# Optimization experiments

Hardware: AMD Instinct MI355X
Metric: run time of the kernel (lower is better)

The kernel has to match this reference:

```python
import jax, jax.numpy as jnp
import numpy as np

N = 100000   # nodes
E = 300000   # directed edges
D = 256      # emb_dim
G = 4000     # graphs
L = 5        # num_layer
F_IN = 40    # num_atom_features
NUM_BOND_TYPE = 6       # pretrain-gnns convention; self-loop bond type = 4
NUM_BOND_DIRECTION = 3
EPS = 1e-5


def setup_inputs() -> dict:
    key = jax.random.key(0)
    ks = jax.random.split(key, 32)
    s = 0.05
    inp = {}
    inp["x"] = jax.random.normal(ks[0], (N, F_IN), jnp.float32)
    inp["edge_index"] = jax.random.randint(ks[1], (2, E), 0, N)
    inp["edge_attr"] = jax.random.randint(ks[2], (E, 2), 0, 3)
    inp["batch"] = jnp.sort(jax.random.randint(ks[3], (N,), 0, G))
    # atom embedding (Linear + ReLU)
    inp["embW"] = jax.random.normal(ks[4], (F_IN, D), jnp.float32) * s
    inp["embB"] = jnp.zeros((D,), jnp.float32)
    # per-layer GINConv params (stacked over layers)
    inp["ee1"] = jax.random.normal(ks[5], (L, NUM_BOND_TYPE, D), jnp.float32) * s
    inp["ee2"] = jax.random.normal(ks[6], (L, NUM_BOND_DIRECTION, D), jnp.float32) * s
    inp["W1"] = jax.random.normal(ks[7], (L, D, 2 * D), jnp.float32) * s
    inp["b1"] = jnp.zeros((L, 2 * D), jnp.float32)
    inp["W2"] = jax.random.normal(ks[8], (L, 2 * D, D), jnp.float32) * s
    inp["b2"] = jnp.zeros((L, D), jnp.float32)
    inp["bn_g"] = jnp.ones((L, D), jnp.float32)
    inp["bn_b"] = jnp.zeros((L, D), jnp.float32)
    # MLP head: 256 -> 256 -> 128 -> 64 -> 32 -> 1
    dims = [D, D, D // 2, D // 4, D // 8]
    kk = jax.random.split(ks[9], 5)
    for i in range(4):
        inp[f"hW{i}"] = jax.random.normal(kk[i], (dims[i], dims[i + 1]), jnp.float32) * s
        inp[f"hb{i}"] = jnp.zeros((dims[i + 1],), jnp.float32)
    inp["hWo"] = jax.random.normal(kk[4], (dims[4], 1), jnp.float32) * s
    inp["hbo"] = jnp.zeros((1,), jnp.float32)
    return inp


def reference(x, edge_index, edge_attr, batch, embW, embB, ee1, ee2, W1, b1, W2, b2,
              bn_g, bn_b, hW0, hb0, hW1, hb1, hW2, hb2, hW3, hb3, hWo, hbo):
    src, dst = edge_index[0], edge_index[1]
    ea0, ea1 = edge_attr[:, 0], edge_attr[:, 1]
    # x_embedding1: Linear + ReLU
    h = jax.nn.relu(x @ embW + embB)
    for l in range(L):
        # GINConv: gather source features + edge embeddings, scatter-add to dst
        msg = h[src] + ee1[l][ea0] + ee2[l][ea1]        # [E, D]
        agg = jax.ops.segment_sum(msg, dst, num_segments=N)
        # self-loop message (bond type 4, direction 0)
        agg = agg + h + ee1[l][4] + ee2[l][0]
        # GIN MLP: Linear(D, 2D) -> ReLU -> Linear(2D, D)
        h2 = jax.nn.relu(agg @ W1[l] + b1[l]) @ W2[l] + b2[l]
        # BatchNorm1d (training-mode batch statistics, biased variance)
        mu = h2.mean(axis=0)
        var = h2.var(axis=0)
        h2 = (h2 - mu) * jax.lax.rsqrt(var + EPS) * bn_g[l] + bn_b[l]
        if l < L - 1:
            h2 = jax.nn.relu(h2)
        # dropout with drop_ratio=0.0 -> identity
        h = h2
    # JK == 'last'
    node_rep = h
    # global_mean_pool
    counts = jnp.maximum(jax.ops.segment_sum(jnp.ones((N,), node_rep.dtype), batch, num_segments=G), 1.0)
    mol = jax.ops.segment_sum(node_rep, batch, num_segments=G) / counts[:, None]
    # MLP head
    z = jax.nn.relu(mol @ hW0 + hb0)
    z = jax.nn.relu(z @ hW1 + hb1)
    z = jax.nn.relu(z @ hW2 + hb2)
    z = jax.nn.relu(z @ hW3 + hb3)
    out = z @ hWo + hbo
    return out.reshape(-1)  # MolEmbed.view(-1), num_tasks == 1
```

## Files before the change

### kernel.cpp

```cpp
#include <hip/hip_runtime.h>
#include <hip/hip_bf16.h>

#define NN 100000
#define EE 300000
#define GG 4000
#define LL 5
#define GPB 4
#define SC_CHUNK 1024
#define SC_NB ((NN + SC_CHUNK - 1) / SC_CHUNK)

typedef _Float16 half8  __attribute__((ext_vector_type(8)));
typedef _Float16 half4v __attribute__((ext_vector_type(4)));
typedef float    f32x4  __attribute__((ext_vector_type(4)));

__device__ inline short f2h(float f) {
    _Float16 h = (_Float16)f;
    short s; __builtin_memcpy(&s, &h, 2); return s;
}

__device__ inline void async_load16(const void* g, void* l) {
    __builtin_amdgcn_global_load_lds(
        (const __attribute__((address_space(1))) unsigned int*)g,
        (__attribute__((address_space(3))) unsigned int*)l, 16, 0, 0);
}

__global__ __launch_bounds__(256) void k_count(
    int* __restrict__ deg, const int* __restrict__ ei)
{
    int e = blockIdx.x * 256 + threadIdx.x;
    if (e < EE) atomicAdd(&deg[ei[EE + e]], 1);
}

__global__ __launch_bounds__(256) void k_scan_partial(
    int* __restrict__ partial, const int* __restrict__ deg)
{
    int b = blockIdx.x, t = threadIdx.x;
    int lane = t & 63, w = t >> 6;
    int base = b * SC_CHUNK + t * 4;
    int s = 0;
#pragma unroll
    for (int j = 0; j < 4; ++j) {
        int i = base + j;
        if (i < NN) s += deg[i];
    }
#pragma unroll
    for (int off = 1; off < 64; off <<= 1) s += __shfl_xor(s, off, 64);
    __shared__ int ws[4];
    if (lane == 0) ws[w] = s;
    __syncthreads();
    if (t == 0) partial[b] = ws[0] + ws[1] + ws[2] + ws[3];
}

__global__ __launch_bounds__(128) void k_scan_base(
    int* __restrict__ bases, int* __restrict__ offs, const int* __restrict__ partial)
{
    int t = threadIdx.x;
    int lane = t & 63, w = t >> 6;
    int p = (t < SC_NB) ? partial[t] : 0;
    int x = p;
#pragma unroll
    for (int off = 1; off < 64; off <<= 1) {
        int nb = __shfl_up(x, off, 64);
        if (lane >= off) x += nb;
    }
    __shared__ int w0tot;
    if (t == 63) w0tot = x;
    __syncthreads();
    if (w == 1) x += w0tot;
    if (t < SC_NB) bases[t] = x - p;
    if (t == 0) offs[NN] = EE;
}

__global__ __launch_bounds__(256) void k_scan_final(
    int* __restrict__ offs, int* __restrict__ cursor,
    const int* __restrict__ deg, const int* __restrict__ bases)
{
    int b = blockIdx.x, t = threadIdx.x;
    int lane = t & 63, w = t >> 6;
    int base = b * SC_CHUNK + t * 4;
    int v[4], pre[4], run = 0;
#pragma unroll
    for (int j = 0; j < 4; ++j) {
        int i = base + j;
        v[j] = (i < NN) ? deg[i] : 0;
        pre[j] = run;
        run += v[j];
    }
    int x = run;
#pragma unroll
    for (int off = 1; off < 64; off <<= 1) {
        int nb = __shfl_up(x, off, 64);
        if (lane >= off) x += nb;
    }
    int tex = x - run;
    __shared__ int ws[4];
    if (lane == 63) ws[w] = x;
    __syncthreads();
    int woff = 0;
    for (int k = 0; k < 4; ++k) if (k < w) woff += ws[k];
    int tbase = bases[b] + woff + tex;
#pragma unroll
    for (int j = 0; j < 4; ++j) {
        int i = base + j;
        if (i < NN) { offs[i] = tbase + pre[j]; cursor[i] = tbase + pre[j]; }
    }
}

__global__ __launch_bounds__(256) void k_fill(
    int* __restrict__ csr, int* __restrict__ cursor,
    const int* __restrict__ ei, const int* __restrict__ ea)
{
    int e = blockIdx.x * 256 + threadIdx.x;
    if (e >= EE) return;
    int s = ei[e];
    int d = ei[EE + e];
    int c = ea[2 * e] * 3 + ea[2 * e + 1];
    int slot = atomicAdd(&cursor[d], 1);
    csr[slot] = s | (c << 20);
}

__global__ __launch_bounds__(256) void k_goffs(
    int* __restrict__ goffs, const int* __restrict__ batch)
{
    int n = blockIdx.x * 256 + threadIdx.x;
    if (n >= NN) return;
    int b = batch[n];
    int bp = (n == 0) ? -1 : batch[n - 1];
    for (int g = bp + 1; g <= b; ++g) goffs[g] = n;
    if (n == NN - 1)
        for (int g = b + 1; g <= GG; ++g) goffs[g] = NN;
}

__global__ __launch_bounds__(256) void k_combo(
    float* __restrict__ tbl, const float* __restrict__ ee1, const float* __restrict__ ee2)
{
    int c = blockIdx.x;
    int l = blockIdx.y;
    int t = threadIdx.x;
    int i1 = (c < 9) ? c / 3 : 4;
    int i2 = (c < 9) ? c % 3 : 0;
    tbl[((size_t)l * 10 + c) * 256 + t] =
        ee1[((size_t)l * 6 + i1) * 256 + t] + ee2[((size_t)l * 3 + i2) * 256 + t];
}

__global__ __launch_bounds__(256) void k_pack_emb(
    _Float16* __restrict__ Wep, const float* __restrict__ embW)
{
    int idx = blockIdx.x * 256 + threadIdx.x;
    int ks = idx >> 13, r = idx & 8191;
    int n = r >> 5, kk = r & 31;
    int k = ks * 32 + kk;
    float v = (k < 40) ? embW[(size_t)k * 256 + n] : 0.f;
    Wep[idx] = (_Float16)v;
}

__global__ __launch_bounds__(256) void k_embed_mfma(
    _Float16* __restrict__ H, const float* __restrict__ x,
    const _Float16* __restrict__ Wep, const float* __restrict__ bias)
{
    __shared__ __align__(16) char smem[67584];
    _Float16* As = (_Float16*)smem;
    _Float16* Bs = (_Float16*)(smem + 16384);
    _Float16* Cs = (_Float16*)smem;

    const int t = threadIdx.x;
    const int w = t >> 6, lane = t & 63;
    const int quad = lane >> 4, l16 = lane & 15;
    const int wr = w >> 1, wc = w & 1;
    const int gm0 = blockIdx.x * 128;

#pragma unroll
    for (int i = 0; i < 8; ++i) {
        int u = i * 256 + t;
        async_load16((const char*)Wep + u * 16, (char*)Bs + u * 16);
    }

    {
        int row = t >> 1, half = t & 1;
        int rg = gm0 + row; if (rg > NN - 1) rg = NN - 1;
        const float* xp = x + (size_t)rg * 40 + half * 20;
        float v[20];
#pragma unroll
        for (int j = 0; j < 5; ++j) {
            float4 q = *(const float4*)(xp + j * 4);
            v[j * 4 + 0] = q.x; v[j * 4 + 1] = q.y; v[j * 4 + 2] = q.z; v[j * 4 + 3] = q.w;
        }
#pragma unroll
        for (int j = 0; j < 20; ++j) {
            int col = half * 20 + j;
            int ks = col >> 5, kk = col & 31;
            As[ks * 4096 + row * 32 + kk] = (_Float16)v[j];
        }
        int kb = 8 + half * 12;
#pragma unroll
        for (int j = 0; j < 12; ++j)
            As[4096 + row * 32 + kb + j] = (_Float16)0.f;
    }

    float biasreg[8];
#pragma unroll
    for (int nt = 0; nt < 8; ++nt)
        biasreg[nt] = bias[wc * 128 + nt * 16 + l16];

    f32x4 acc[4][8];
#pragma unroll
    for (int i = 0; i < 4; ++i)
#pragma unroll
        for (int j = 0; j < 8; ++j) acc[i][j] = (f32x4){0.f, 0.f, 0.f, 0.f};

    __syncthreads();

#pragma unroll
    for (int ks = 0; ks < 2; ++ks) {
        half8 af[4], bfr[8];
#pragma unroll
        for (int mt = 0; mt < 4; ++mt)
            af[mt] = *(const half8*)(As + ks * 4096 + (wr * 64 + mt * 16 + l16) * 32 + quad * 8);
#pragma unroll
        for (int nt = 0; nt < 8; ++nt)
            bfr[nt] = *(const half8*)(Bs + ks * 8192 + (wc * 128 + nt * 16 + l16) * 32 + quad * 8);
#pragma unroll
        for (int mt = 0; mt < 4; ++mt)
#pragma unroll
            for (int nt = 0; nt < 8; ++nt)
                acc[mt][nt] = __builtin_amdgcn_mfma_f32_16x16x32_f16(
                    af[mt], bfr[nt], acc[mt][nt], 0, 0, 0);
    }

    __syncthreads();
#pragma unroll
    for (int mt = 0; mt < 4; ++mt)
#pragma unroll
        for (int nt = 0; nt < 8; ++nt)
#pragma unroll
            for (int r = 0; r < 4; ++r) {
                int row = wr * 64 + mt * 16 + quad * 4 + r;
                int col = wc * 128 + nt * 16 + l16;
                Cs[row * 264 + col] = (_Float16)fmaxf(acc[mt][nt][r] + biasreg[nt], 0.f);
            }
    __syncthreads();
#pragma unroll
    for (int i = 0; i < 16; ++i) {
        int u = i * 256 + t;
        int m = u >> 5, ch = u & 31;
        int grow = gm0 + m;
        if (grow < NN)
            *(int4*)(H + (size_t)grow * 256 + ch * 8) =
                *(const int4*)(Cs + m * 264 + ch * 8);
    }
}

template <int AFF>
__global__ __launch_bounds__(256) void k_aggregate(
    _Float16* __restrict__ agg, const _Float16* __restrict__ hin,
    const int* __restrict__ offs, const int* __restrict__ csr,
    const float* __restrict__ tbl,
    const float* __restrict__ scale, const float* __restrict__ shift)
{
    int t = threadIdx.x;
    int w = t >> 6, lane = t & 63;
    int n = blockIdx.x * 4 + w;

    f32x4 sc, sh;
    if (AFF) { sc = ((const f32x4*)scale)[lane]; sh = ((const f32x4*)shift)[lane]; }
    const f32x4* tb4 = (const f32x4*)tbl;

    half4v hv = *(const half4v*)(hin + (size_t)n * 256 + lane * 4);
    f32x4 acc = tb4[9 * 64 + lane];
#pragma unroll
    for (int i = 0; i < 4; ++i) {
        float v = (float)hv[i];
        if (AFF) v = fmaf(v, sc[i], sh[i]);
        acc[i] += fmaxf(v, 0.f);
    }

    int o0 = offs[n], o1 = offs[n + 1];
    for (int j = o0; j < o1; ++j) {
        int entry = csr[j];
        int s = entry & 0xFFFFF;
        int c = entry >> 20;
        half4v gv = *(const half4v*)(hin + (size_t)s * 256 + lane * 4);
        f32x4 tv = tb4[c * 64 + lane];
#pragma unroll
        for (int i = 0; i < 4; ++i) {
            float v = (float)gv[i];
            if (AFF) v = fmaf(v, sc[i], sh[i]);
            acc[i] += fmaxf(v, 0.f) + tv[i];
        }
    }

    half4v o;
#pragma unroll
    for (int i = 0; i < 4; ++i) o[i] = (_Float16)acc[i];
    *(half4v*)(agg + (size_t)n * 256 + lane * 4) = o;
}

__global__ __launch_bounds__(256) void k_pack(
    short* __restrict__ dst, const float* __restrict__ src, int K, int Nsz)
{
    int nb = blockIdx.x, kb = blockIdx.y, l = blockIdx.z;
    int t = threadIdx.x;
    __shared__ float T[32][65];
    const float* s = src + ((size_t)l * K + kb * 32) * Nsz + nb * 64;
#pragma unroll
    for (int i = 0; i < 8; ++i) {
        int idx = i * 256 + t;
        int kk = idx >> 6, nl = idx & 63;
        T[kk][nl] = s[(size_t)kk * Nsz + nl];
    }
    __syncthreads();
    int nl = t >> 2, kq = t & 3;
    union { short s[8]; int4 v; } o;
#pragma unroll
    for (int j = 0; j < 8; ++j) o.s[j] = f2h(T[kq * 8 + j][nl]);
    short* d = dst + (((size_t)l * (K / 32) + kb) * Nsz + nb * 64 + nl) * 32 + kq * 8;
    *(int4*)d = o.v;
}

__global__ __launch_bounds__(256, 3) void k_fused_mlp(
    _Float16* __restrict__ H2, const _Float16* __restrict__ A,
    const short* __restrict__ W1p, const float* __restrict__ b1,
    const short* __restrict__ W2p, const float* __restrict__ b2,
    float* __restrict__ stats)
{
    __shared__ __align__(16) char smem[49152];
    _Float16* As = (_Float16*)smem;
    _Float16* Us = (_Float16*)(smem + 32768);
    _Float16* Cs = (_Float16*)smem;

    const int t = threadIdx.x;
    const int w = t >> 6, lane = t & 63;
    const int quad = lane >> 4, l16 = lane & 15;
    const int bm = blockIdx.x;
    const int gm0 = bm * 64;
    const int swz = l16 & 7;

#pragma unroll
    for (int i = 0; i < 8; ++i) {
        int u = i * 256 + t;
        int row = u >> 5;
        int gcol = (u & 31) ^ (row & 7);
        int grow = gm0 + row; if (grow > NN - 1) grow = NN - 1;
        async_load16(A + (size_t)grow * 256 + gcol * 8, (char*)As + u * 16);
    }

    const _Float16* w1w = (const _Float16*)W1p + ((size_t)(w * 32 + l16)) * 32 + quad * 8;
    const _Float16* w2w = (const _Float16*)W2p + ((size_t)(w * 64 + l16)) * 32 + quad * 8;

    half8 a1p[2];
#pragma unroll
    for (int ct = 0; ct < 2; ++ct)
        a1p[ct] = *(const half8*)(w1w + (size_t)(ct * 16) * 32);

    f32x4 acc2[4][4];
#pragma unroll
    for (int i = 0; i < 4; ++i)
#pragma unroll
        for (int j = 0; j < 4; ++j) acc2[i][j] = (f32x4){0.f, 0.f, 0.f, 0.f};

    __syncthreads();

    for (int j = 0; j < 4; ++j) {
        f32x4 acc1[2][4];
#pragma unroll
        for (int a = 0; a < 2; ++a)
#pragma unroll
            for (int b = 0; b < 4; ++b) acc1[a][b] = (f32x4){0.f, 0.f, 0.f, 0.f};

#pragma unroll
        for (int kb = 0; kb < 8; ++kb) {
            half8 a1c[2];
            a1c[0] = a1p[0]; a1c[1] = a1p[1];
            if (kb < 7) {
#pragma unroll
                for (int ct = 0; ct < 2; ++ct)
                    a1p[ct] = *(const half8*)(w1w +
                        ((size_t)(kb + 1) * 512 + j * 128 + ct * 16) * 32);
            }
            int slotA = (kb * 4 + quad) ^ swz;
            half8 b1f[4];
#pragma unroll
            for (int urt = 0; urt < 4; ++urt)
                b1f[urt] = *(const half8*)(As + (urt * 16 + l16) * 256 + slotA * 8);
#pragma unroll
            for (int ct = 0; ct < 2; ++ct)
#pragma unroll
                for (int urt = 0; urt < 4; ++urt)
                    acc1[ct][urt] = __builtin_amdgcn_mfma_f32_16x16x32_f16(
                        a1c[ct], b1f[urt], acc1[ct][urt], 0, 0, 0);
        }

        half8 a2p[4];
#pragma unroll
        for (int nt = 0; nt < 4; ++nt)
            a2p[nt] = *(const half8*)(w2w + ((size_t)(j * 4) * 256 + nt * 16) * 32);

#pragma unroll
        for (int ct = 0; ct < 2; ++ct) {
            int ucl = w * 32 + ct * 16 + quad * 4;
            float4 bv = *(const float4*)(b1 + j * 128 + ucl);
            int G = ucl >> 3;
            int hs = quad & 1;
#pragma unroll
            for (int urt = 0; urt < 4; ++urt) {
                int ur = urt * 16 + l16;
                int S = G ^ (ur & 7);
                half4v o;
                o[0] = (_Float16)fmaxf(acc1[ct][urt][0] + bv.x, 0.f);
                o[1] = (_Float16)fmaxf(acc1[ct][urt][1] + bv.y, 0.f);
                o[2] = (_Float16)fmaxf(acc1[ct][urt][2] + bv.z, 0.f);
                o[3] = (_Float16)fmaxf(acc1[ct][urt][3] + bv.w, 0.f);
                *(half4v*)(Us + ur * 128 + S * 8 + hs * 4) = o;
            }
        }
        asm volatile("s_waitcnt lgkmcnt(0)" ::: "memory");
        __builtin_amdgcn_s_barrier();
        __builtin_amdgcn_sched_barrier(0);

#pragma unroll
        for (int kk = 0; kk < 4; ++kk) {
            half8 a2c[4];
#pragma unroll
            for (int nt = 0; nt < 4; ++nt) a2c[nt] = a2p[nt];
            if (kk < 3) {
#pragma unroll
                for (int nt = 0; nt < 4; ++nt)
                    a2p[nt] = *(const half8*)(w2w +
                        ((size_t)(j * 4 + kk + 1) * 256 + nt * 16) * 32);
            } else if (j < 3) {
#pragma unroll
                for (int ct = 0; ct < 2; ++ct)
                    a1p[ct] = *(const half8*)(w1w +
                        ((size_t)(j + 1) * 128 + ct * 16) * 32);
            }
            int slotU = (kk * 4 + quad) ^ swz;
            half8 b2f[4];
#pragma unroll
            for (int mt = 0; mt < 4; ++mt)
                b2f[mt] = *(const half8*)(Us + (mt * 16 + l16) * 128 + slotU * 8);
#pragma unroll
            for (int nt = 0; nt < 4; ++nt)
#pragma unroll
                for (int mt = 0; mt < 4; ++mt)
                    acc2[nt][mt] = __builtin_amdgcn_mfma_f32_16x16x32_f16(
                        a2c[nt], b2f[mt], acc2[nt][mt], 0, 0, 0);
        }
        asm volatile("s_waitcnt lgkmcnt(0)" ::: "memory");
        __builtin_amdgcn_s_barrier();
        __builtin_amdgcn_sched_barrier(0);
    }

    int slot2 = bm & 63;
#pragma unroll
    for (int nt = 0; nt < 4; ++nt) {
        int nb = w * 64 + nt * 16 + quad * 4;
        float4 bv = *(const float4*)(b2 + nb);
        float s1[4] = {0.f, 0.f, 0.f, 0.f};
        float s2[4] = {0.f, 0.f, 0.f, 0.f};
#pragma unroll
        for (int mt = 0; mt < 4; ++mt) {
            int mr = mt * 16 + l16;
            int m = gm0 + mr;
            float v0 = acc2[nt][mt][0] + bv.x;
            float v1 = acc2[nt][mt][1] + bv.y;
            float v2 = acc2[nt][mt][2] + bv.z;
            float v3 = acc2[nt][mt][3] + bv.w;
            half4v o;
            o[0] = (_Float16)v0; o[1] = (_Float16)v1;
            o[2] = (_Float16)v2; o[3] = (_Float16)v3;
            *(half4v*)(Cs + mr * 264 + nb) = o;
            if (m < NN) {
                s1[0] += v0; s1[1] += v1; s1[2] += v2; s1[3] += v3;
                s2[0] += v0 * v0; s2[1] += v1 * v1;
                s2[2] += v2 * v2; s2[3] += v3 * v3;
            }
        }
#pragma unroll
        for (int r = 0; r < 4; ++r) {
            s1[r] += __shfl_xor(s1[r], 1, 64); s2[r] += __shfl_xor(s2[r], 1, 64);
            s1[r] += __shfl_xor(s1[r], 2, 64); s2[r] += __shfl_xor(s2[r], 2, 64);
            s1[r] += __shfl_xor(s1[r], 4, 64); s2[r] += __shfl_xor(s2[r], 4, 64);
            s1[r] += __shfl_xor(s1[r], 8, 64); s2[r] += __shfl_xor(s2[r], 8, 64);
            if (l16 == 0) {
                atomicAdd(&stats[slot2 * 512 + nb + r], s1[r]);
                atomicAdd(&stats[slot2 * 512 + 256 + nb + r], s2[r]);
            }
        }
    }
    __syncthreads();
#pragma unroll
    for (int i = 0; i < 8; ++i) {
        int u = i * 256 + t;
        int m = u >> 5, ch = u & 31;
        int grow = gm0 + m;
        if (grow < NN)
            *(int4*)(H2 + (size_t)grow * 256 + ch * 8) =
                *(const int4*)(Cs + m * 264 + ch * 8);
    }
}

__global__ __launch_bounds__(256) void k_bn_finalize(
    float* __restrict__ scale, float* __restrict__ shift,
    float* __restrict__ stats,
    const float* __restrict__ bn_g, const float* __restrict__ bn_b)
{
    int t = threadIdx.x;
    float s1 = 0.f, s2 = 0.f;
    for (int j = 0; j < 64; ++j) {
        s1 += stats[j * 512 + t];
        s2 += stats[j * 512 + 256 + t];
        stats[j * 512 + t] = 0.f;
        stats[j * 512 + 256 + t] = 0.f;
    }
    float mu  = s1 / (float)NN;
    float var = s2 / (float)NN - mu * mu;
    float sc  = bn_g[t] * rsqrtf(var + 1e-5f);
    scale[t] = sc;
    shift[t] = bn_b[t] - mu * sc;
}

__global__ __launch_bounds__(256) void k_pool(
    float* __restrict__ mol, const _Float16* __restrict__ h,
    const int* __restrict__ goffs,
    const float* __restrict__ scale, const float* __restrict__ shift)
{
    int g = blockIdx.x;
    int t = threadIdx.x;
    int s = goffs[g], e = goffs[g + 1];
    float sum = 0.f;
    for (int n = s; n < e; ++n) sum += (float)h[(size_t)n * 256 + t];
    int c = e - s; if (c < 1) c = 1;
    mol[(size_t)g * 256 + t] = fmaf(sum / (float)c, scale[t], shift[t]);
}

__global__ __launch_bounds__(256) void k_head(
    float* __restrict__ out, const float* __restrict__ mol,
    const float* __restrict__ hW0, const float* __restrict__ hb0,
    const float* __restrict__ hW1, const float* __restrict__ hb1,
    const float* __restrict__ hW2, const float* __restrict__ hb2,
    const float* __restrict__ hW3, const float* __restrict__ hb3,
    const float* __restrict__ hWo, const float* __restrict__ hbo)
{
    __shared__ float za[GPB][256];
    __shared__ float zb[GPB][256];
    const int t = threadIdx.x;
    const int g0 = blockIdx.x * GPB;

#pragma unroll
    for (int g = 0; g < GPB; ++g)
        za[g][t] = mol[(size_t)(g0 + g) * 256 + t];
    __syncthreads();

    {
        float acc[GPB];
#pragma unroll
        for (int g = 0; g < GPB; ++g) acc[g] = 0.f;
        for (int k = 0; k < 256; ++k) {
            float w = hW0[k * 256 + t];
#pragma unroll
            for (int g = 0; g < GPB; ++g) acc[g] = fmaf(za[g][k], w, acc[g]);
        }
        float b = hb0[t];
#pragma unroll
        for (int g = 0; g < GPB; ++g) zb[g][t] = fmaxf(acc[g] + b, 0.f);
    }
    __syncthreads();

    if (t < 128) {
        float acc[GPB];
#pragma unroll
        for (int g = 0; g < GPB; ++g) acc[g] = 0.f;
        for (int k = 0; k < 256; ++k) {
            float w = hW1[k * 128 + t];
#pragma unroll
            for (int g = 0; g < GPB; ++g) acc[g] = fmaf(zb[g][k], w, acc[g]);
        }
        float b = hb1[t];
#pragma unroll
        for (int g = 0; g < GPB; ++g) za[g][t] = fmaxf(acc[g] + b, 0.f);
    }
    __syncthreads();

    if (t < 64) {
        float acc[GPB];
#pragma unroll
        for (int g = 0; g < GPB; ++g) acc[g] = 0.f;
        for (int k = 0; k < 128; ++k) {
            float w = hW2[k * 64 + t];
#pragma unroll
            for (int g = 0; g < GPB; ++g) acc[g] = fmaf(za[g][k], w, acc[g]);
        }
        float b = hb2[t];
#pragma unroll
        for (int g = 0; g < GPB; ++g) zb[g][t] = fmaxf(acc[g] + b, 0.f);
    }
    __syncthreads();

    if (t < 32) {
        float acc[GPB];
#pragma unroll
        for (int g = 0; g < GPB; ++g) acc[g] = 0.f;
        for (int k = 0; k < 64; ++k) {
            float w = hW3[k * 32 + t];
#pragma unroll
            for (int g = 0; g < GPB; ++g) acc[g] = fmaf(zb[g][k], w, acc[g]);
        }
        float b = hb3[t];
#pragma unroll
        for (int g = 0; g < GPB; ++g) za[g][t] = fmaxf(acc[g] + b, 0.f);
    }
    __syncthreads();

    if (t < GPB) {
        float s = hbo[0];
        for (int k = 0; k < 32; ++k) s = fmaf(za[t][k], hWo[k], s);
        out[g0 + t] = s;
    }
}

extern "C" void kernel_launch(void* const* d_in, const int* in_sizes, int n_in,
                              void* d_out, int out_size, void* d_ws, size_t ws_size,
                              hipStream_t stream)
{
    const float* x    = (const float*)d_in[0];
    const int*   ei   = (const int*)d_in[1];
    const int*   ea   = (const int*)d_in[2];
    const int*   batch= (const int*)d_in[3];
    const float* embW = (const float*)d_in[4];
    const float* embB = (const float*)d_in[5];
    const float* ee1  = (const float*)d_in[6];
    const float* ee2  = (const float*)d_in[7];
    const float* W1   = (const float*)d_in[8];
    const float* b1   = (const float*)d_in[9];
    const float* W2   = (const float*)d_in[10];
    const float* b2   = (const float*)d_in[11];
    const float* bng  = (const float*)d_in[12];
    const float* bnb  = (const float*)d_in[13];
    const float* hW0  = (const float*)d_in[14];
    const float* hb0  = (const float*)d_in[15];
    const float* hW1  = (const float*)d_in[16];
    const float* hb1  = (const float*)d_in[17];
    const float* hW2  = (const float*)d_in[18];
    const float* hb2  = (const float*)d_in[19];
    const float* hW3  = (const float*)d_in[20];
    const float* hb3  = (const float*)d_in[21];
    const float* hWo  = (const float*)d_in[22];
    const float* hbo  = (const float*)d_in[23];
    float* out = (float*)d_out;

    char* ws = (char*)d_ws;
    size_t off = 0;
    _Float16* h2buf = (_Float16*)(ws + off); off += (size_t)NN * 256 * 2;
    _Float16* aggbuf= (_Float16*)(ws + off); off += (size_t)NN * 256 * 2;
    short* W1p      = (short*)(ws + off);    off += (size_t)5 * 131072 * 2;
    short* W2p      = (short*)(ws + off);    off += (size_t)5 * 131072 * 2;
    _Float16* Wep   = (_Float16*)(ws + off); off += (size_t)2 * 8192 * 2;
    float* tbl      = (float*)(ws + off);    off += (size_t)5 * 10 * 256 * 4;
    float* stats    = (float*)(ws + off);    off += (size_t)64 * 512 * 4;
    float* scale    = (float*)(ws + off);    off += 256 * 4;
    float* shift    = (float*)(ws + off);    off += 256 * 4;
    float* mol      = (float*)(ws + off);    off += (size_t)GG * 256 * 4;
    int* deg        = (int*)(ws + off);      off += (size_t)NN * 4;
    int* offs       = (int*)(ws + off);      off += (size_t)(NN + 1) * 4;
    int* cursor     = (int*)(ws + off);      off += (size_t)NN * 4;
    int* csr        = (int*)(ws + off);      off += (size_t)EE * 4;
    int* goffs      = (int*)(ws + off);      off += (size_t)(GG + 1) * 4;
    int* partial    = (int*)(ws + off);      off += 128 * 4;
    int* bases      = (int*)(ws + off);      off += 128 * 4;

    hipMemsetAsync(deg, 0, (size_t)NN * 4, stream);
    hipMemsetAsync(stats, 0, (size_t)64 * 512 * 4, stream);
    k_count<<<(EE + 255) / 256, 256, 0, stream>>>(deg, ei);
    k_scan_partial<<<SC_NB, 256, 0, stream>>>(partial, deg);
    k_scan_base<<<1, 128, 0, stream>>>(bases, offs, partial);
    k_scan_final<<<SC_NB, 256, 0, stream>>>(offs, cursor, deg, bases);
    k_fill<<<(EE + 255) / 256, 256, 0, stream>>>(csr, cursor, ei, ea);
    k_goffs<<<(NN + 255) / 256, 256, 0, stream>>>(goffs, batch);
    k_combo<<<dim3(10, 5), 256, 0, stream>>>(tbl, ee1, ee2);
    k_pack<<<dim3(8, 8, 5), 256, 0, stream>>>(W1p, W1, 256, 512);
    k_pack<<<dim3(4, 16, 5), 256, 0, stream>>>(W2p, W2, 512, 256);
    k_pack_emb<<<64, 256, 0, stream>>>(Wep, embW);

    k_embed_mfma<<<782, 256, 0, stream>>>(h2buf, x, Wep, embB);

    const int FB = (NN + 63) / 64;
    for (int l = 0; l < LL; ++l) {
        if (l == 0)
            k_aggregate<0><<<NN / 4, 256, 0, stream>>>(aggbuf, h2buf, offs, csr,
                                                       tbl, scale, shift);
        else
            k_aggregate<1><<<NN / 4, 256, 0, stream>>>(aggbuf, h2buf, offs, csr,
                                                       tbl + (size_t)l * 10 * 256, scale, shift);
        k_fused_mlp<<<FB, 256, 0, stream>>>(h2buf, aggbuf,
                                            W1p + (size_t)l * 131072, b1 + l * 512,
                                            W2p + (size_t)l * 131072, b2 + l * 256, stats);
        k_bn_finalize<<<1, 256, 0, stream>>>(scale, shift, stats, bng + l * 256, bnb + l * 256);
    }

    k_pool<<<GG, 256, 0, stream>>>(mol, h2buf, goffs, scale, shift);
    k_head<<<GG / GPB, 256, 0, stream>>>(out, mol,
                                         hW0, hb0, hW1, hb1, hW2, hb2, hW3, hb3, hWo, hbo);
}
```

Baseline: 998.9 us.

## Fuse neighbor aggregation into the GIN MLP kernel, writing straight to LDS

The separate aggregation kernel is removed. Each MLP block now gathers and sums neighbor messages for its own 64 rows and writes the fp16 result directly into the swizzled shared-memory A tile. This drops the global round trip of the aggregated tensor and one launch per layer, and the layer input and output now ping-pong between two buffers. The risk is that the gather runs inside a kernel limited to 3 blocks per CU with a heavy register footprint, so latency hiding for the irregular loads may suffer. The serial 16-row loop per wave also adds imbalance from varying node degree.

```diff
diff --git a/kernel.cpp b/kernel.cpp
--- a/kernel.cpp
+++ b/kernel.cpp
@@ -250,51 +250,6 @@
     }
 }
 
-template <int AFF>
-__global__ __launch_bounds__(256) void k_aggregate(
-    _Float16* __restrict__ agg, const _Float16* __restrict__ hin,
-    const int* __restrict__ offs, const int* __restrict__ csr,
-    const float* __restrict__ tbl,
-    const float* __restrict__ scale, const float* __restrict__ shift)
-{
-    int t = threadIdx.x;
-    int w = t >> 6, lane = t & 63;
-    int n = blockIdx.x * 4 + w;
-
-    f32x4 sc, sh;
-    if (AFF) { sc = ((const f32x4*)scale)[lane]; sh = ((const f32x4*)shift)[lane]; }
-    const f32x4* tb4 = (const f32x4*)tbl;
-
-    half4v hv = *(const half4v*)(hin + (size_t)n * 256 + lane * 4);
-    f32x4 acc = tb4[9 * 64 + lane];
-#pragma unroll
-    for (int i = 0; i < 4; ++i) {
-        float v = (float)hv[i];
-        if (AFF) v = fmaf(v, sc[i], sh[i]);
-        acc[i] += fmaxf(v, 0.f);
-    }
-
-    int o0 = offs[n], o1 = offs[n + 1];
-    for (int j = o0; j < o1; ++j) {
-        int entry = csr[j];
-        int s = entry & 0xFFFFF;
-        int c = entry >> 20;
-        half4v gv = *(const half4v*)(hin + (size_t)s * 256 + lane * 4);
-        f32x4 tv = tb4[c * 64 + lane];
-#pragma unroll
-        for (int i = 0; i < 4; ++i) {
-            float v = (float)gv[i];
-            if (AFF) v = fmaf(v, sc[i], sh[i]);
-            acc[i] += fmaxf(v, 0.f) + tv[i];
-        }
-    }
-
-    half4v o;
-#pragma unroll
-    for (int i = 0; i < 4; ++i) o[i] = (_Float16)acc[i];
-    *(half4v*)(agg + (size_t)n * 256 + lane * 4) = o;
-}
-
 __global__ __launch_bounds__(256) void k_pack(
     short* __restrict__ dst, const float* __restrict__ src, int K, int Nsz)
 {
@@ -317,8 +272,12 @@
     *(int4*)d = o.v;
 }
 
-__global__ __launch_bounds__(256, 3) void k_fused_mlp(
-    _Float16* __restrict__ H2, const _Float16* __restrict__ A,
+template <int AFF>
+__global__ __launch_bounds__(256, 3) void k_fused_layer(
+    _Float16* __restrict__ H2, const _Float16* __restrict__ Hprev,
+    const int* __restrict__ offs, const int* __restrict__ csr,
+    const float* __restrict__ tbl,
+    const float* __restrict__ scale, const float* __restrict__ shift,
     const short* __restrict__ W1p, const float* __restrict__ b1,
     const short* __restrict__ W2p, const float* __restrict__ b2,
     float* __restrict__ stats)
@@ -335,13 +294,42 @@
     const int gm0 = bm * 64;
     const int swz = l16 & 7;
 
-#pragma unroll
-    for (int i = 0; i < 8; ++i) {
-        int u = i * 256 + t;
-        int row = u >> 5;
-        int gcol = (u & 31) ^ (row & 7);
-        int grow = gm0 + row; if (grow > NN - 1) grow = NN - 1;
-        async_load16(A + (size_t)grow * 256 + gcol * 8, (char*)As + u * 16);
+    {
+        f32x4 sc, sh;
+        if (AFF) { sc = ((const f32x4*)scale)[lane]; sh = ((const f32x4*)shift)[lane]; }
+        const f32x4* tb4 = (const f32x4*)tbl;
+        const int g9 = lane >> 1, hs2 = lane & 1;
+        for (int i = 0; i < 16; ++i) {
+            int r = w * 16 + i;
+            int n = gm0 + r; if (n > NN - 1) n = NN - 1;
+            f32x4 acc = tb4[9 * 64 + lane];
+            half4v hv = *(const half4v*)(Hprev + (size_t)n * 256 + lane * 4);
+#pragma unroll
+            for (int q = 0; q < 4; ++q) {
+                float v = (float)hv[q];
+                if (AFF) v = fmaf(v, sc[q], sh[q]);
+                acc[q] += fmaxf(v, 0.f);
+            }
+            int o0 = offs[n], o1 = offs[n + 1];
+            for (int e = o0; e < o1; ++e) {
+                int entry = csr[e];
+                int s = entry & 0xFFFFF;
+                int c = entry >> 20;
+                half4v gv = *(const half4v*)(Hprev + (size_t)s * 256 + lane * 4);
+                f32x4 tv = tb4[c * 64 + lane];
+#pragma unroll
+                for (int q = 0; q < 4; ++q) {
+                    float v = (float)gv[q];
+                    if (AFF) v = fmaf(v, sc[q], sh[q]);
+                    acc[q] += fmaxf(v, 0.f) + tv[q];
+                }
+            }
+            half4v o;
+#pragma unroll
+            for (int q = 0; q < 4; ++q) o[q] = (_Float16)acc[q];
+            int slot = g9 ^ (r & 7);
+            *(half4v*)(As + r * 256 + slot * 8 + hs2 * 4) = o;
+        }
     }
 
     const _Float16* w1w = (const _Float16*)W1p + ((size_t)(w * 32 + l16)) * 32 + quad * 8;
@@ -358,7 +346,9 @@
 #pragma unroll
         for (int j = 0; j < 4; ++j) acc2[i][j] = (f32x4){0.f, 0.f, 0.f, 0.f};
 
-    __syncthreads();
+    asm volatile("s_waitcnt lgkmcnt(0)" ::: "memory");
+    __builtin_amdgcn_s_barrier();
+    __builtin_amdgcn_sched_barrier(0);
 
     for (int j = 0; j < 4; ++j) {
         f32x4 acc1[2][4];
@@ -683,21 +673,24 @@
 
     k_embed_mfma<<<782, 256, 0, stream>>>(h2buf, x, Wep, embB);
 
+    _Float16* hb[2] = { h2buf, aggbuf };
     const int FB = (NN + 63) / 64;
     for (int l = 0; l < LL; ++l) {
+        _Float16* src = hb[l & 1];
+        _Float16* dst = hb[(l + 1) & 1];
         if (l == 0)
-            k_aggregate<0><<<NN / 4, 256, 0, stream>>>(aggbuf, h2buf, offs, csr,
-                                                       tbl, scale, shift);
+            k_fused_layer<0><<<FB, 256, 0, stream>>>(dst, src, offs, csr,
+                tbl, scale, shift,
+                W1p, b1, W2p, b2, stats);
         else
-            k_aggregate<1><<<NN / 4, 256, 0, stream>>>(aggbuf, h2buf, offs, csr,
-                                                       tbl + (size_t)l * 10 * 256, scale, shift);
-        k_fused_mlp<<<FB, 256, 0, stream>>>(h2buf, aggbuf,
-                                            W1p + (size_t)l * 131072, b1 + l * 512,
-                                            W2p + (size_t)l * 131072, b2 + l * 256, stats);
+            k_fused_layer<1><<<FB, 256, 0, stream>>>(dst, src, offs, csr,
+                tbl + (size_t)l * 10 * 256, scale, shift,
+                W1p + (size_t)l * 131072, b1 + l * 512,
+                W2p + (size_t)l * 131072, b2 + l * 256, stats);
         k_bn_finalize<<<1, 256, 0, stream>>>(scale, shift, stats, bng + l * 256, bnb + l * 256);
     }
 
-    k_pool<<<GG, 256, 0, stream>>>(mol, h2buf, goffs, scale, shift);
+    k_pool<<<GG, 256, 0, stream>>>(mol, hb[LL & 1], goffs, scale, shift);
     k_head<<<GG / GPB, 256, 0, stream>>>(out, mol,
                                          hW0, hb0, hW1, hb1, hW2, hb2, hW3, hb3, hWo, hbo);
 }
```

Measured after the change: 1.107 ms. 1.11x slower.
